# Kernel optimization log

Measured on AMD Instinct MI355X. Metric: run time of the kernel, lower is better.

Reference implementation:

```python
import jax, jax.numpy as jnp
import numpy as np

# dims: B batch, CIN/COUT channels, K kernel, H/W spatial, S stride, P padding
B, CIN, COUT, K, H, W, S, P = 8, 16, 64, 3, 32, 32, 1, 1
ALPHA, R, N_EKV, VT, VD = 0.05625, 0.1, 1.5, 0.025, 0.1


def setup_inputs() -> dict:
    key = jax.random.key(0)
    k1, k2 = jax.random.split(key)
    x = jax.random.normal(k1, (B, CIN, H, W), dtype=jnp.float32)
    # torch init: uniform_(theta, 1.0, 8.0)
    theta = jax.random.uniform(k2, (COUT, CIN * K * K), dtype=jnp.float32, minval=1.0, maxval=8.0)
    scale = jnp.array(1.0, dtype=jnp.float32)
    return {"x": x, "theta": theta, "scale": scale}


def _unfold(x, k, s, p):
    # torch.nn.Unfold: patches flattened channel-major as (C, kh, kw)
    b, c, h, w = x.shape
    ho = (h + 2 * p - k) // s + 1
    wo = (w + 2 * p - k) // s + 1
    xp = jnp.pad(x, ((0, 0), (0, 0), (p, p), (p, p)))
    patches = jnp.stack(
        [xp[:, :, i:i + ho * s:s, j:j + wo * s:s] for i in range(k) for j in range(k)],
        axis=2,
    )  # (B, C, K*K, Ho, Wo)
    return patches.reshape(b, c * k * k, ho * wo), ho, wo


def _log1p_exp_stable_sq(a):
    # clamp to [-50, 20] then softplus; squared (EKV f)
    a = jnp.clip(a, -50.0, 20.0)
    sp = jnp.log1p(jnp.exp(a))
    return sp * sp


def reference(x, theta, scale):
    theta = jnp.clip(theta, 1.0, 8.0)  # mirrors theta.data.clamp_(1, 8)
    vg, ho, wo = _unfold(x, K, S, P)          # (B, Cin*K^2, L)
    vg = vg[:, None, :, :]                    # (B, 1, Cin*K^2, L)
    vth = theta[None, :, :, None]             # (1, Cout, Cin*K^2, 1)
    denom = 2.0 * N_EKV * VT
    term1 = _log1p_exp_stable_sq((vg - vth) / denom)
    term2 = _log1p_exp_stable_sq((vg - vth - VD) / denom)
    currents = jnp.clip(ALPHA * (term1 - term2), 0.0, None)
    i_k = jnp.sum(currents, axis=2)           # reduce over Cin*K^2 -> (B, Cout, L)
    v_out = i_k * R * scale
    return v_out.reshape(x.shape[0], COUT, ho, wo)
```

## Files before the change

kernel.cpp:

```cpp
#include <hip/hip_runtime.h>

#define BB 8
#define CIN 16
#define COUT 64
#define HH 32
#define WW 32
#define PH 34
#define PW 34
#define PPLANE (PH * PW)

#define SCALE_C 19.235933878519388f
#define K2V (SCALE_C * 0.1f)
#define B_HI 28.85390081777927f
#define WINLO_S (-13.849872392533959f)
#define OUT_CONST (0.4804530139182014f * 0.05625f * 0.1f)

#define EXP2F(x) __builtin_amdgcn_exp2f(x)
#define LOG2F(x) __builtin_amdgcn_logf(x)

#define TAB_H (SCALE_C / 320.0f)
#define TAB_INVH (320.0f / SCALE_C)
#define TAB_OFF 234.0f
#define TAB_UMAX 746.5f
#define TAB_LAST 746
#define TAB_N 752

#define NTH (COUT * CIN * 9)

__global__ __launch_bounds__(256) void init_kernel(const float* __restrict__ x,
                                                   const float* __restrict__ theta,
                                                   float* __restrict__ xp,
                                                   float* __restrict__ thp) {
    if (blockIdx.x < 578) {
        int idx = blockIdx.x * 256 + threadIdx.x;
        int c = idx / PPLANE;
        int r = idx - c * PPLANE;
        int y = r / PW;
        int xc = r - y * PW;
        float v = 0.0f;
        if (y >= 1 && y <= HH && xc >= 1 && xc <= WW) {
            v = x[c * (HH * WW) + (y - 1) * WW + (xc - 1)] * SCALE_C;
        }
        xp[idx] = v;
    } else {
        int i = (blockIdx.x - 578) * 256 + threadIdx.x;
        if (i < NTH) {
            thp[i] = fminf(fmaxf(theta[i], 1.0f), 8.0f) * SCALE_C;
        }
    }
}

__device__ __forceinline__ void load9(const float* __restrict__ p, float* v) {
#pragma unroll
    for (int dy = 0; dy < 3; ++dy)
#pragma unroll
        for (int dx = 0; dx < 3; ++dx)
            v[dy * 3 + dx] = p[dy * PW + dx];
}

__device__ __forceinline__ void compute9(const float* v, const float* __restrict__ thp,
                                         const float* __restrict__ T, float* acc) {
#pragma unroll
    for (int k = 0; k < 9; ++k) {
        float b1 = v[k] - thp[k];
        if (__any(b1 > WINLO_S)) {
            float u = fmaf(b1, TAB_INVH, TAB_OFF);
            u = fminf(fmaxf(u, 0.0f), TAB_UMAX);
            float fi = floorf(u);
            float fr = u - fi;
            int i = (int)fi;
            float t0 = T[i];
            float t1 = T[i + 1];
            float a = acc[k % 3];
            a += fmaf(fr, t1 - t0, t0);
            acc[k % 3] = a;
        }
    }
}

__global__ __launch_bounds__(256, 8) void ekv_kernel(const float* __restrict__ xp,
                                                     const float* __restrict__ thp,
                                                     const float* __restrict__ scale,
                                                     float* __restrict__ out) {
    __shared__ float T[TAB_N];
    for (int i = threadIdx.x; i < TAB_N; i += 256) {
        float val = 0.0f;
        if (i <= TAB_LAST) {
            float b1 = ((float)i - TAB_OFF) * TAB_H;
            float e1 = EXP2F(b1);
            float l1 = fminf(LOG2F(1.0f + e1), B_HI);
            float e2 = EXP2F(b1 - K2V);
            float l2 = fminf(LOG2F(1.0f + e2), B_HI);
            val = fmaf(l1, l1, -(l2 * l2));
        }
        T[i] = val;
    }
    __syncthreads();

    int bid = blockIdx.x;
    int b = bid & 7;
    int tile = (bid >> 3) & 3;
    int cl = (bid >> 5) & 7;
    int cm = bid >> 8;
    int co = cm * 8 + cl;

    int t = threadIdx.x;
    int ow = t & 31;
    int oh = tile * 8 + (t >> 5);

    const float* thc = thp + co * (CIN * 9);
    const float* p0 = xp + (size_t)b * (CIN * PPLANE) + oh * PW + ow;

    float acc[3] = {0.0f, 0.0f, 0.0f};

    float va[9], vb[9];
    load9(p0, va);
#pragma unroll 1
    for (int cin = 0; cin < CIN; cin += 2) {
        load9(p0 + (cin + 1) * PPLANE, vb);
        compute9(va, thc + cin * 9, T, acc);
        int nc = cin + 2 < CIN ? cin + 2 : CIN - 1;
        load9(p0 + nc * PPLANE, va);
        compute9(vb, thc + (cin + 1) * 9, T, acc);
    }

    float sc = scale[0] * (OUT_CONST);
    out[(((size_t)b * COUT + co) * HH + oh) * WW + ow] =
        (acc[0] + acc[1] + acc[2]) * sc;
}

extern "C" void kernel_launch(void* const* d_in, const int* in_sizes, int n_in,
                              void* d_out, int out_size, void* d_ws, size_t ws_size,
                              hipStream_t stream) {
    const float* x = (const float*)d_in[0];
    const float* theta = (const float*)d_in[1];
    const float* scale = (const float*)d_in[2];
    float* out = (float*)d_out;

    float* thp = (float*)d_ws;
    float* xp = thp + NTH;
    (void)ws_size;

    init_kernel<<<578 + (NTH + 255) / 256, 256, 0, stream>>>(x, theta, xp, thp);
    ekv_kernel<<<BB * 4 * COUT, 256, 0, stream>>>(xp, thp, scale, out);
}
```

Measured before the change: 73.83 us.

## Fuse padding and theta preprocessing into main EKV kernel

```diff
diff --git a/kernel.cpp b/kernel.cpp
--- a/kernel.cpp
+++ b/kernel.cpp
@@ -5,15 +5,13 @@
 #define COUT 64
 #define HH 32
 #define WW 32
-#define PH 34
-#define PW 34
-#define PPLANE (PH * PW)
 
 #define SCALE_C 19.235933878519388f
 #define K2V (SCALE_C * 0.1f)
 #define B_HI 28.85390081777927f
 #define WINLO_S (-13.849872392533959f)
 #define OUT_CONST (0.4804530139182014f * 0.05625f * 0.1f)
+#define VNEG (-1.0e4f)
 
 #define EXP2F(x) __builtin_amdgcn_exp2f(x)
 #define LOG2F(x) __builtin_amdgcn_logf(x)
@@ -25,44 +23,22 @@
 #define TAB_LAST 746
 #define TAB_N 752
 
-#define NTH (COUT * CIN * 9)
-
-__global__ __launch_bounds__(256) void init_kernel(const float* __restrict__ x,
-                                                   const float* __restrict__ theta,
-                                                   float* __restrict__ xp,
-                                                   float* __restrict__ thp) {
-    if (blockIdx.x < 578) {
-        int idx = blockIdx.x * 256 + threadIdx.x;
-        int c = idx / PPLANE;
-        int r = idx - c * PPLANE;
-        int y = r / PW;
-        int xc = r - y * PW;
-        float v = 0.0f;
-        if (y >= 1 && y <= HH && xc >= 1 && xc <= WW) {
-            v = x[c * (HH * WW) + (y - 1) * WW + (xc - 1)] * SCALE_C;
-        }
-        xp[idx] = v;
-    } else {
-        int i = (blockIdx.x - 578) * 256 + threadIdx.x;
-        if (i < NTH) {
-            thp[i] = fminf(fmaxf(theta[i], 1.0f), 8.0f) * SCALE_C;
-        }
-    }
+__device__ __forceinline__ void load9g(const float* __restrict__ p, const int* off9,
+                                       float* v) {
+#pragma unroll
+    for (int k = 0; k < 9; ++k) v[k] = p[off9[k]];
 }
 
-__device__ __forceinline__ void load9(const float* __restrict__ p, float* v) {
+__device__ __forceinline__ void compute9(const float* v, const float* __restrict__ TH,
+                                         int cin, const bool* val9,
+                                         const float* __restrict__ T, float* acc) {
+    float th9[9];
 #pragma unroll
-    for (int dy = 0; dy < 3; ++dy)
-#pragma unroll
-        for (int dx = 0; dx < 3; ++dx)
-            v[dy * 3 + dx] = p[dy * PW + dx];
-}
-
-__device__ __forceinline__ void compute9(const float* v, const float* __restrict__ thp,
-                                         const float* __restrict__ T, float* acc) {
+    for (int k = 0; k < 9; ++k) th9[k] = TH[cin * 9 + k];
 #pragma unroll
     for (int k = 0; k < 9; ++k) {
-        float b1 = v[k] - thp[k];
+        float b1 = fmaf(v[k], SCALE_C, -th9[k]);
+        b1 = val9[k] ? b1 : VNEG;
         if (__any(b1 > WINLO_S)) {
             float u = fmaf(b1, TAB_INVH, TAB_OFF);
             u = fminf(fmaxf(u, 0.0f), TAB_UMAX);
@@ -78,12 +54,23 @@
     }
 }
 
-__global__ __launch_bounds__(256, 8) void ekv_kernel(const float* __restrict__ xp,
-                                                     const float* __restrict__ thp,
-                                                     const float* __restrict__ scale,
-                                                     float* __restrict__ out) {
+__global__ __launch_bounds__(256, 8) void ekv_fused(const float* __restrict__ x,
+                                                    const float* __restrict__ theta,
+                                                    const float* __restrict__ scale,
+                                                    float* __restrict__ out) {
     __shared__ float T[TAB_N];
-    for (int i = threadIdx.x; i < TAB_N; i += 256) {
+    __shared__ float TH[CIN * 9];
+
+    int bid = blockIdx.x;
+    int b = bid & 7;
+    int tile = (bid >> 3) & 3;
+    int cl = (bid >> 5) & 7;
+    int cm = bid >> 8;
+    int co = cm * 8 + cl;
+
+    int t = threadIdx.x;
+
+    for (int i = t; i < TAB_N; i += 256) {
         float val = 0.0f;
         if (i <= TAB_LAST) {
             float b1 = ((float)i - TAB_OFF) * TAB_H;
@@ -95,33 +82,48 @@
         }
         T[i] = val;
     }
+    if (t < CIN * 9) {
+        TH[t] = fminf(fmaxf(theta[co * (CIN * 9) + t], 1.0f), 8.0f) * SCALE_C;
+    }
     __syncthreads();
 
-    int bid = blockIdx.x;
-    int b = bid & 7;
-    int tile = (bid >> 3) & 3;
-    int cl = (bid >> 5) & 7;
-    int cm = bid >> 8;
-    int co = cm * 8 + cl;
-
-    int t = threadIdx.x;
     int ow = t & 31;
     int oh = tile * 8 + (t >> 5);
 
-    const float* thc = thp + co * (CIN * 9);
-    const float* p0 = xp + (size_t)b * (CIN * PPLANE) + oh * PW + ow;
+    int yoff[3], col[3];
+    bool vy[3], vx[3];
+#pragma unroll
+    for (int d = 0; d < 3; ++d) {
+        int y = oh - 1 + d;
+        vy[d] = ((unsigned)y < HH);
+        yoff[d] = (y < 0 ? 0 : (y > HH - 1 ? HH - 1 : y)) * WW;
+        int c = ow - 1 + d;
+        vx[d] = ((unsigned)c < WW);
+        col[d] = (c < 0 ? 0 : (c > WW - 1 ? WW - 1 : c));
+    }
+    int off9[9];
+    bool val9[9];
+#pragma unroll
+    for (int dy = 0; dy < 3; ++dy)
+#pragma unroll
+        for (int dx = 0; dx < 3; ++dx) {
+            off9[dy * 3 + dx] = yoff[dy] + col[dx];
+            val9[dy * 3 + dx] = vy[dy] && vx[dx];
+        }
+
+    const float* xb = x + (size_t)b * (CIN * HH * WW);
 
     float acc[3] = {0.0f, 0.0f, 0.0f};
 
     float va[9], vb[9];
-    load9(p0, va);
+    load9g(xb, off9, va);
 #pragma unroll 1
     for (int cin = 0; cin < CIN; cin += 2) {
-        load9(p0 + (cin + 1) * PPLANE, vb);
-        compute9(va, thc + cin * 9, T, acc);
+        load9g(xb + (cin + 1) * (HH * WW), off9, vb);
+        compute9(va, TH, cin, val9, T, acc);
         int nc = cin + 2 < CIN ? cin + 2 : CIN - 1;
-        load9(p0 + nc * PPLANE, va);
-        compute9(vb, thc + (cin + 1) * 9, T, acc);
+        load9g(xb + nc * (HH * WW), off9, va);
+        compute9(vb, TH, cin + 1, val9, T, acc);
     }
 
     float sc = scale[0] * (OUT_CONST);
@@ -136,11 +138,8 @@
     const float* theta = (const float*)d_in[1];
     const float* scale = (const float*)d_in[2];
     float* out = (float*)d_out;
-
-    float* thp = (float*)d_ws;
-    float* xp = thp + NTH;
+    (void)d_ws;
     (void)ws_size;
 
-    init_kernel<<<578 + (NTH + 255) / 256, 256, 0, stream>>>(x, theta, xp, thp);
-    ekv_kernel<<<BB * 4 * COUT, 256, 0, stream>>>(xp, thp, scale, out);
+    ekv_fused<<<BB * 4 * COUT, 256, 0, stream>>>(x, theta, scale, out);
 }
```

Measured after the change: 74.36 us. Within noise of the previous version (+0.7%).
